# Kernel optimization log

Hardware: AMD Instinct MI355X
Metric: run time of the kernel (lower is better)

Reference implementation:

```python
import jax, jax.numpy as jnp
import numpy as np

B, OBS, H, D, E, T, A = 8192, 128, 512, 512, 16, 50, 32
LOG_STD_MIN, LOG_STD_MAX = -20.0, 2.0
ACT_LIMIT = 1.0


def setup_inputs() -> dict:
    key = jax.random.key(0)
    ks = jax.random.split(key, 24)
    s = 0.05  # weight init scale for MLP weights
    f32 = jnp.float32
    return {
        "obs": jax.random.normal(ks[0], (B, OBS), f32),
        "task": jax.random.randint(ks[1], (B,), 0, T),
        "eps": jax.random.normal(ks[2], (B, A), f32),
        # backbone: obs_dim -> 512 -> 512, relu after every layer
        "bW1": jax.random.normal(ks[3], (OBS, H), f32) * s, "bb1": jnp.zeros((H,), f32),
        "bW2": jax.random.normal(ks[4], (H, H), f32) * s, "bb2": jnp.zeros((H,), f32),
        # stacked expert MLPs: 512 -> 512(relu) -> 512(identity), batched over E
        "eW1": jax.random.normal(ks[5], (E, H, D), f32) * s, "eb1": jnp.zeros((E, D), f32),
        "eW2": jax.random.normal(ks[6], (E, D, D), f32) * s, "eb2": jnp.zeros((E, D), f32),
        # attention params (torch.randn init in original)
        "key_mats": jax.random.normal(ks[7], (E, D, D), f32),
        "value_mats": jax.random.normal(ks[8], (E, D, D), f32),
        "task_queries": jax.random.normal(ks[9], (T, D), f32),
        # mu tower: D -> 512(relu) -> act_dim
        "mW1": jax.random.normal(ks[10], (D, H), f32) * s, "mb1": jnp.zeros((H,), f32),
        "mW2": jax.random.normal(ks[11], (H, A), f32) * s, "mb2": jnp.zeros((A,), f32),
        # log_std tower: D -> 512(relu) -> act_dim
        "lW1": jax.random.normal(ks[12], (D, H), f32) * s, "lb1": jnp.zeros((H,), f32),
        "lW2": jax.random.normal(ks[13], (H, A), f32) * s, "lb2": jnp.zeros((A,), f32),
    }


def reference(obs, task, eps, bW1, bb1, bW2, bb2, eW1, eb1, eW2, eb2,
              key_mats, value_mats, task_queries,
              mW1, mb1, mW2, mb2, lW1, lb1, lW2, lb2):
    relu = jax.nn.relu
    # backbone (relu after both layers, incl. output_activation=activation)
    h = relu(obs @ bW1 + bb1)          # [B, H]
    h = relu(h @ bW2 + bb2)            # [B, H]
    # all experts as one batched GEMM (replaces jit.fork per-expert dispatch)
    eo = relu(jnp.einsum('bi,eij->bej', h, eW1) + eb1)   # [B, E, D]
    eo = jnp.einsum('bej,ejk->bek', eo, eW2) + eb2       # [B, E, D]
    # attention-weighted mixture of experts
    vals = jnp.einsum('bei,eij->bej', eo, value_mats)    # [B, E, D]
    keys = jnp.einsum('bei,eij->bej', eo, key_mats)      # [B, E, D]
    q = task_queries[task]                               # [B, D]
    w = jax.nn.softmax(jnp.einsum('bei,bi->be', keys, q), axis=-1)  # [B, E]
    tower = jnp.einsum('be,bei->bi', w, vals)            # [B, D]
    # squashed Gaussian head
    mu = relu(tower @ mW1 + mb1) @ mW2 + mb2             # [B, A]
    log_std = jnp.clip(relu(tower @ lW1 + lb1) @ lW2 + lb2, LOG_STD_MIN, LOG_STD_MAX)
    a = mu + jnp.exp(log_std) * eps                      # rsample with explicit noise
    # Normal log_prob of a = mu + std*eps, summed over action dim
    logp = jnp.sum(-0.5 * eps * eps - log_std - 0.5 * jnp.log(2.0 * jnp.pi), axis=-1)
    # tanh-squash correction
    logp = logp - jnp.sum(2.0 * (jnp.log(2.0) - a - jax.nn.softplus(-2.0 * a)), axis=-1)
    pi = ACT_LIMIT * jnp.tanh(a)
    return (pi, logp)
```

## Files before the change

kernel.cpp:

```cpp
#include <hip/hip_runtime.h>
#include <hip/hip_bf16.h>
#include <cstdint>


typedef _Float16 f16;
typedef _Float16 f16x4 __attribute__((ext_vector_type(4)));
typedef _Float16 f16x8 __attribute__((ext_vector_type(8)));
typedef float f32x4 __attribute__((ext_vector_type(4)));

__device__ __forceinline__ void fsplit(float x, f16& h, f16& l) {
    h = (f16)x;
    l = (f16)(x - (float)h);
}

__device__ __forceinline__ void gload16(const void* g, void* s) {
    __builtin_amdgcn_global_load_lds(
        (const __attribute__((address_space(1))) void*)g,
        (__attribute__((address_space(3))) void*)s, 16, 0, 0);
}

__global__ void split_pairs(const float* __restrict__ x, f16* __restrict__ h,
                            f16* __restrict__ l, int n4) {
    int i = blockIdx.x * 256 + threadIdx.x;
    if (i >= n4) return;
    float4 v = ((const float4*)x)[i];
    float a[4] = {v.x, v.y, v.z, v.w};
    f16x4 hh, ll;
#pragma unroll
    for (int j = 0; j < 4; ++j) { f16 hj, lj; fsplit(a[j], hj, lj); hh[j] = hj; ll[j] = lj; }
    *(f16x4*)&h[(long)i * 4] = hh;
    *(f16x4*)&l[(long)i * 4] = ll;
}

__global__ void transpose_split(const float* __restrict__ W, f16* __restrict__ Th,
                                f16* __restrict__ Tl, int K, int N, long ist, long ost) {
    __shared__ float t[32][33];
    const float* Wb = W + (long)blockIdx.z * ist;
    const int k0 = blockIdx.x * 32, n0 = blockIdx.y * 32;
    const int tid = threadIdx.x;
    const int r = tid >> 3, c4 = (tid & 7) * 4;
    float4 v = *(const float4*)&Wb[(long)(k0 + r) * N + n0 + c4];
    t[r][c4] = v.x; t[r][c4 + 1] = v.y; t[r][c4 + 2] = v.z; t[r][c4 + 3] = v.w;
    __syncthreads();
    f16x4 hh, ll;
#pragma unroll
    for (int j = 0; j < 4; ++j) { f16 hj, lj; fsplit(t[c4 + j][r], hj, lj); hh[j] = hj; ll[j] = lj; }
    long ob = (long)blockIdx.z * ost + (long)(n0 + r) * K + k0 + c4;
    *(f16x4*)&Th[ob] = hh;
    *(f16x4*)&Tl[ob] = ll;
}

__global__ void build_w2t(const float* __restrict__ mW2, const float* __restrict__ lW2,
                          float* __restrict__ W2T) {
    const int i = blockIdx.x * 256 + threadIdx.x;
    const int half = i >> 14, col = (i >> 9) & 31, k = i & 511;
    const float* src = half ? lW2 : mW2;
    W2T[i] = src[k * 32 + col];
}

__global__ void build_bcat(const float* __restrict__ mb1, const float* __restrict__ lb1,
                           float* __restrict__ bcat) {
    const int i = blockIdx.x * 256 + threadIdx.x;
    bcat[i] = (i < 512) ? mb1[i] : lb1[i - 512];
}

template <int OUTM, bool RELU, int AMODE, bool BSINGLE>
__global__ __launch_bounds__(256, AMODE == 0 ? 3 : 4) void gemm_pair(
    const f16* __restrict__ Ah, const f16* __restrict__ Al, int lda, long zsA,
    const f16* __restrict__ Bh, const f16* __restrict__ Bl, int ldb, long zsB,
    const float* __restrict__ bias, long zsBias,
    f16* __restrict__ Ch, f16* __restrict__ Cl, float* __restrict__ Cf,
    int ldc, long zsC, int K,
    const float* __restrict__ wscale,
    const int* __restrict__ task, const float* __restrict__ KQ2,
    float* __restrict__ scores) {
    __shared__ f16 As[AMODE == 0 ? 2 : 1][64][64];
    __shared__ f16 Bs[BSINGLE ? 1 : 2][128][64];
    const int z = blockIdx.z;
    Ah += (long)z * zsA;
    if constexpr (AMODE == 0) Al += (long)z * zsA;
    Bh += (long)z * zsB;
    if constexpr (!BSINGLE) Bl += (long)z * zsB;
    if (bias) bias += (long)z * zsBias;
    if (OUTM <= 1) { Ch += (long)z * zsC; Cl += (long)z * zsC; }
    if (OUTM == 7) { Ch += (long)z * zsC; }
    if (OUTM == 2 || OUTM == 3 || OUTM == 6) { Cf += (long)z * zsC; }
    const int tid = threadIdx.x;
    const int l = tid & 63;
    const int w = tid >> 6;
    const int row0 = blockIdx.x * 64;
    const int col0 = blockIdx.y * 128;
    const int wr = (w >> 1) * 32;
    const int wc = (w & 1) * 64;
    const int grow = l >> 3;
    const int gch = (l & 7) ^ grow;

    f32x4 acc[2][4];
#pragma unroll
    for (int mi = 0; mi < 2; ++mi)
#pragma unroll
        for (int ni = 0; ni < 4; ++ni)
#pragma unroll
            for (int j = 0; j < 4; ++j) acc[mi][ni][j] = 0.f;

    uint4 areg0, areg1; float ascl0, ascl1;
    auto ldA = [&](int k0) {
        const int r0 = w * 16 + grow, r1 = r0 + 8;
        const int scl = l & 7;
        areg0 = *(const uint4*)&Ah[(long)(row0 + r0) * lda + k0 + scl * 8];
        areg1 = *(const uint4*)&Ah[(long)(row0 + r1) * lda + k0 + scl * 8];
        const int e = k0 >> 9;
        ascl0 = wscale[(long)(row0 + r0) * 16 + e];
        ascl1 = wscale[(long)(row0 + r1) * 16 + e];
    };
    auto wrA = [&]() {
        const int scl = l & 7;
#pragma unroll
        for (int h = 0; h < 2; ++h) {
            const int r = w * 16 + grow + h * 8;
            const float s = h ? ascl1 : ascl0;
            f16x8 v = h ? *(f16x8*)&areg1 : *(f16x8*)&areg0;
#pragma unroll
            for (int j = 0; j < 8; ++j) v[j] = (f16)((float)v[j] * s);
            *(uint4*)&As[0][r][(scl ^ (r & 7)) * 8] = *(uint4*)&v;
        }
    };

    if constexpr (AMODE == 2) ldA(0);
    for (int k0 = 0; k0 < K; k0 += 64) {
        __syncthreads();
        if constexpr (AMODE == 2) {
            wrA();
            if (k0 + 64 < K) ldA(k0 + 64);
        } else {
            const long ga = (long)(row0 + w * 16 + grow) * lda + k0 + gch * 8;
            gload16(Ah + ga, &As[0][w * 16][0]);
            gload16(Ah + ga + (long)8 * lda, &As[0][w * 16 + 8][0]);
            if constexpr (AMODE == 0) {
                gload16(Al + ga, &As[1][w * 16][0]);
                gload16(Al + ga + (long)8 * lda, &As[1][w * 16 + 8][0]);
            }
        }
        {
            const long gb = (long)(col0 + w * 32 + grow) * ldb + k0 + gch * 8;
            gload16(Bh + gb, &Bs[0][w * 32][0]);
            gload16(Bh + gb + (long)8 * ldb, &Bs[0][w * 32 + 8][0]);
            gload16(Bh + gb + (long)16 * ldb, &Bs[0][w * 32 + 16][0]);
            gload16(Bh + gb + (long)24 * ldb, &Bs[0][w * 32 + 24][0]);
            if constexpr (!BSINGLE) {
                gload16(Bl + gb, &Bs[1][w * 32][0]);
                gload16(Bl + gb + (long)8 * ldb, &Bs[1][w * 32 + 8][0]);
                gload16(Bl + gb + (long)16 * ldb, &Bs[1][w * 32 + 16][0]);
                gload16(Bl + gb + (long)24 * ldb, &Bs[1][w * 32 + 24][0]);
            }
        }
        __syncthreads();
        const int r16 = l & 15, kg = l >> 4;
#pragma unroll
        for (int ks = 0; ks < 2; ++ks) {
            f16x8 a_h[2], a_l[2], b_h[4], b_l[4];
#pragma unroll
            for (int mi = 0; mi < 2; ++mi) {
                const int r = wr + mi * 16 + r16;
                const int off = ((ks * 4 + kg) ^ (r & 7)) * 8;
                a_h[mi] = *(const f16x8*)&As[0][r][off];
                if constexpr (AMODE == 0) a_l[mi] = *(const f16x8*)&As[1][r][off];
            }
#pragma unroll
            for (int ni = 0; ni < 4; ++ni) {
                const int c = wc + ni * 16 + r16;
                const int off = ((ks * 4 + kg) ^ (c & 7)) * 8;
                b_h[ni] = *(const f16x8*)&Bs[0][c][off];
                if constexpr (!BSINGLE) b_l[ni] = *(const f16x8*)&Bs[1][c][off];
            }
#pragma unroll
            for (int mi = 0; mi < 2; ++mi)
#pragma unroll
                for (int ni = 0; ni < 4; ++ni) {
                    acc[mi][ni] = __builtin_amdgcn_mfma_f32_16x16x32_f16(a_h[mi], b_h[ni], acc[mi][ni], 0, 0, 0);
                    if constexpr (!BSINGLE)
                        acc[mi][ni] = __builtin_amdgcn_mfma_f32_16x16x32_f16(a_h[mi], b_l[ni], acc[mi][ni], 0, 0, 0);
                    if constexpr (AMODE == 0)
                        acc[mi][ni] = __builtin_amdgcn_mfma_f32_16x16x32_f16(a_l[mi], b_h[ni], acc[mi][ni], 0, 0, 0);
                }
        }
    }
    const int lane15 = l & 15;
    const int rsub = (l >> 4) * 4;
    if (OUTM == 5) {
        const int expert = col0 >> 9;
        float bv[4];
#pragma unroll
        for (int ni = 0; ni < 4; ++ni)
            bv[ni] = bias ? bias[col0 + wc + ni * 16 + lane15] : 0.f;
#pragma unroll
        for (int mi = 0; mi < 2; ++mi)
#pragma unroll
            for (int j = 0; j < 4; ++j) {
                const int rowg = row0 + wr + mi * 16 + rsub + j;
                const int t = task[rowg];
                const float* kqr = KQ2 + ((long)t * 16 + expert) * 512;
                float part = 0.f;
#pragma unroll
                for (int ni = 0; ni < 4; ++ni) {
                    const int colg = col0 + wc + ni * 16 + lane15;
                    float v = acc[mi][ni][j] + bv[ni];
                    if (RELU) v = fmaxf(v, 0.f);
                    Ch[(long)rowg * ldc + colg] = (f16)v;
                    part += v * kqr[colg & 511];
                }
#pragma unroll
                for (int d = 1; d < 16; d <<= 1) part += __shfl_xor(part, d);
                if (lane15 == 0) atomicAdd(&scores[rowg * 16 + expert], part);
            }
    } else {
#pragma unroll
        for (int mi = 0; mi < 2; ++mi)
#pragma unroll
            for (int ni = 0; ni < 4; ++ni) {
                const int colg = col0 + wc + ni * 16 + lane15;
                const float bv = bias ? bias[colg] : 0.f;
#pragma unroll
                for (int j = 0; j < 4; ++j) {
                    const int rowg = row0 + wr + mi * 16 + rsub + j;
                    float v = acc[mi][ni][j] + bv;
                    if (RELU) v = fmaxf(v, 0.f);
                    if (OUTM == 0) {
                        f16 hh, ll; fsplit(v, hh, ll);
                        const long idx = (long)rowg * ldc + colg;
                        Ch[idx] = hh; Cl[idx] = ll;
                    } else if (OUTM == 1) {
                        f16 hh, ll; fsplit(v, hh, ll);
                        const long idx = (long)colg * ldc + rowg;
                        Ch[idx] = hh; Cl[idx] = ll;
                    } else if (OUTM == 2) {
                        Cf[(long)rowg * ldc + colg] = v;
                    } else if (OUTM == 3) {
                        Cf[(long)rowg * ldc + colg] += v;
                    } else if (OUTM == 6) {
                        Cf[(long)colg * ldc + rowg] = v;
                    } else if (OUTM == 7) {
                        Ch[(long)colg * ldc + rowg] = (f16)v;
                    } else if (OUTM == 8) {
                        const long idx = (long)rowg * ldc + colg;
                        v += Cf[idx];
                        Ch[idx] = (f16)v;
                    }
                }
            }
    }
}

__global__ void cb_from_kq(const f16* __restrict__ KqT_h, const f16* __restrict__ KqT_l,
                           const float* __restrict__ eb2, float* __restrict__ cb) {
    const int gw = (blockIdx.x * 256 + threadIdx.x) >> 6;
    const int l = threadIdx.x & 63;
    const int t = gw >> 4, e = gw & 15;
    const long base = (long)t * 8192 + e * 512 + l * 8;
    f16x8 hh = *(const f16x8*)&KqT_h[base];
    f16x8 ll = *(const f16x8*)&KqT_l[base];
    const float* bb = eb2 + e * 512 + l * 8;
    float s = 0.f;
#pragma unroll
    for (int j = 0; j < 8; ++j) s += ((float)hh[j] + (float)ll[j]) * bb[j];
#pragma unroll
    for (int d = 1; d < 64; d <<= 1) s += __shfl_xor(s, d);
    if (l == 0) cb[t * 16 + e] = s;
}

__global__ void bias_fold(const float* __restrict__ bvec, const float* __restrict__ M,
                          float* __restrict__ out) {
    const int gid = blockIdx.x * 256 + threadIdx.x;
    const int e = gid >> 9, j = gid & 511;
    const float* Me = M + (long)e * 262144;
    const float* be = bvec + e * 512;
    float s = 0.f;
    for (int k = 0; k < 512; ++k) s += be[k] * Me[(long)k * 512 + j];
    out[gid] = s;
}

__global__ void scores_init(const int* __restrict__ task, const float* __restrict__ cb,
                            float* __restrict__ sc) {
    const int i = blockIdx.x * 256 + threadIdx.x;
    sc[i] = cb[task[i >> 4] * 16 + (i & 15)];
}

__global__ void softmax16(float* __restrict__ sc) {
    const int b = blockIdx.x * 256 + threadIdx.x;
    float v[16];
    const float4* pp = (const float4*)&sc[b * 16];
#pragma unroll
    for (int qq = 0; qq < 4; ++qq) {
        float4 t = pp[qq];
        v[qq * 4] = t.x; v[qq * 4 + 1] = t.y; v[qq * 4 + 2] = t.z; v[qq * 4 + 3] = t.w;
    }
    float m = v[0];
#pragma unroll
    for (int e = 1; e < 16; ++e) m = fmaxf(m, v[e]);
    float ssum = 0.f;
#pragma unroll
    for (int e = 0; e < 16; ++e) { v[e] = expf(v[e] - m); ssum += v[e]; }
    const float inv = 1.f / ssum;
    float4* o = (float4*)&sc[b * 16];
#pragma unroll
    for (int qq = 0; qq < 4; ++qq) {
        float4 t;
        t.x = v[qq * 4] * inv; t.y = v[qq * 4 + 1] * inv;
        t.z = v[qq * 4 + 2] * inv; t.w = v[qq * 4 + 3] * inv;
        o[qq] = t;
    }
}

__global__ void wb_init(const float* __restrict__ w, const float* __restrict__ b2V,
                        float* __restrict__ towerAcc) {
    const int b = blockIdx.x;
    const int tid = threadIdx.x;
    float wv[16];
#pragma unroll
    for (int e = 0; e < 16; ++e) wv[e] = w[b * 16 + e];
#pragma unroll
    for (int rep = 0; rep < 2; ++rep) {
        const int j = rep * 256 + tid;
        float s = 0.f;
#pragma unroll
        for (int e = 0; e < 16; ++e) s += wv[e] * b2V[e * 512 + j];
        towerAcc[(long)b * 512 + j] = s;
    }
}

__global__ void head_kernel2(
    const f16* __restrict__ Rh, const f16* __restrict__ Rl,
    const float* __restrict__ W2T,
    const float* __restrict__ mb2, const float* __restrict__ lb2,
    const float* __restrict__ eps, float* __restrict__ pi, float* __restrict__ logp) {
    __shared__ float src[4][1032];
    const int tid = threadIdx.x, l = tid & 63, w = tid >> 6;
    const int b = blockIdx.x * 4 + w;
    const long rb = (long)b * 1024;
    {
        f16x8 h0 = *(const f16x8*)&Rh[rb + l * 8];
        f16x8 l0 = *(const f16x8*)&Rl[rb + l * 8];
        f16x8 h1 = *(const f16x8*)&Rh[rb + 512 + l * 8];
        f16x8 l1 = *(const f16x8*)&Rl[rb + 512 + l * 8];
#pragma unroll
        for (int j = 0; j < 8; ++j) {
            src[w][l * 8 + j] = (float)h0[j] + (float)l0[j];
            src[w][512 + l * 8 + j] = (float)h1[j] + (float)l1[j];
        }
    }
    __syncthreads();
    const int col = l & 31;
    const int half = l >> 5;
    const float4* wp = (const float4*)(W2T + ((long)(half * 32 + col)) * 512);
    const float4* sp = (const float4*)(&src[w][half * 512]);
    float a0 = 0.f, a1 = 0.f, a2 = 0.f, a3 = 0.f;
#pragma unroll 8
    for (int k4 = 0; k4 < 128; ++k4) {
        const float4 wv = wp[k4];
        const float4 sv = sp[k4];
        a0 = fmaf(wv.x, sv.x, a0);
        a1 = fmaf(wv.y, sv.y, a1);
        a2 = fmaf(wv.z, sv.z, a2);
        a3 = fmaf(wv.w, sv.w, a3);
    }
    const float* b2 = half ? lb2 : mb2;
    float s = b2[col] + ((a0 + a1) + (a2 + a3));
    const float other = __shfl_xor(s, 32);
    if (half == 0) {
        const float mu = s;
        float ls = fminf(fmaxf(other, -20.f), 2.f);
        const float e = eps[(long)b * 32 + col];
        const float a = mu + expf(ls) * e;
        float lt = -0.5f * e * e - ls - 0.91893853320467274f;
        const float x = -2.f * a;
        const float sp2 = fmaxf(x, 0.f) + log1pf(expf(-fabsf(x)));
        lt -= 2.f * (0.69314718055994531f - a - sp2);
        pi[(long)b * 32 + col] = tanhf(a);
        float r = lt;
#pragma unroll
        for (int d = 1; d < 32; d <<= 1) r += __shfl_xor(r, d);
        if (col == 0) logp[b] = r;
    }
}

extern "C" void kernel_launch(void* const* d_in, const int* in_sizes, int n_in,
                              void* d_out, int out_size, void* d_ws, size_t ws_size,
                              hipStream_t stream) {
    const float* obs = (const float*)d_in[0];
    const int* task = (const int*)d_in[1];
    const float* eps = (const float*)d_in[2];
    const float* bW1 = (const float*)d_in[3];
    const float* bb1 = (const float*)d_in[4];
    const float* bW2 = (const float*)d_in[5];
    const float* bb2 = (const float*)d_in[6];
    const float* eW1 = (const float*)d_in[7];
    const float* eb1 = (const float*)d_in[8];
    const float* eW2 = (const float*)d_in[9];
    const float* eb2 = (const float*)d_in[10];
    const float* keyM = (const float*)d_in[11];
    const float* valM = (const float*)d_in[12];
    const float* tq = (const float*)d_in[13];
    const float* mW1 = (const float*)d_in[14];
    const float* mb1 = (const float*)d_in[15];
    const float* mW2 = (const float*)d_in[16];
    const float* mb2 = (const float*)d_in[17];
    const float* lW1 = (const float*)d_in[18];
    const float* lb1 = (const float*)d_in[19];
    const float* lW2 = (const float*)d_in[20];
    const float* lb2 = (const float*)d_in[21];
    (void)in_sizes; (void)n_in; (void)out_size; (void)ws_size;

    const size_t MB = 1u << 20, KB = 1u << 10;
    char* base = (char*)d_ws;
    f16* eW1t_h = (f16*)(base + 0 * MB);   f16* eW1t_l = (f16*)(base + 8 * MB);
    f16* Wv2_h  = (f16*)(base + 16 * MB);
    f16* eW2s_h = (f16*)(base + 32 * MB);  f16* eW2s_l = (f16*)(base + 40 * MB);
    f16* h2_h   = (f16*)(base + 32 * MB);  f16* h2_l   = (f16*)(base + 40 * MB);
    f16* t1_h   = (f16*)(base + 48 * MB);  f16* t1_l   = (f16*)(base + 56 * MB);
    f16* Rcat_l = (f16*)(base + 48 * MB);
    f16* Vt_h   = (f16*)(base + 64 * MB);  f16* Vt_l   = (f16*)(base + 72 * MB);
    f16* Rcat_h = (f16*)(base + 64 * MB);
    f16* keyMs_h = (f16*)(base + 80 * MB); f16* keyMs_l = (f16*)(base + 88 * MB);
    f16* KqT_h   = (f16*)(base + 96 * MB); f16* KqT_l   = (f16*)(base + 98 * MB);
    f16* tqP_h   = (f16*)(base + 100 * MB); f16* tqP_l  = (f16*)(base + 100 * MB + 128 * KB);
    float* KQ2   = (float*)(base + 104 * MB);
    float* towerAcc = (float*)(base + 80 * MB);
    f16* twP_h  = (f16*)(base + 96 * MB);
    f16* obs_h  = (f16*)(base + 112 * MB); f16* obs_l  = (f16*)(base + 114 * MB);
    char* q = base + 116 * MB;
    f16* bW1t_h = (f16*)q; q += 128 * KB;  f16* bW1t_l = (f16*)q; q += 128 * KB;
    f16* bW2t_h = (f16*)q; q += 512 * KB;  f16* bW2t_l = (f16*)q; q += 512 * KB;
    f16* mW1t_h = (f16*)q; q += 512 * KB;
    f16* lW1t_h = (f16*)q; q += 512 * KB;
    f16* mW1t_l = (f16*)q; q += 512 * KB;
    f16* lW1t_l = (f16*)q; q += 512 * KB;
    float* scores = (float*)q; q += 512 * KB;
    float* b2V    = (float*)q; q += 32 * KB;
    float* cb     = (float*)q; q += 16 * KB;
    float* W2T    = (float*)q; q += 128 * KB;
    float* bcat   = (float*)q; q += 16 * KB;
    f16* U = (f16*)(base + 122 * MB);

    const long EST = 262144;

    split_pairs<<<1024, 256, 0, stream>>>(obs, obs_h, obs_l, 262144);
    split_pairs<<<4096, 256, 0, stream>>>(eW2, eW2s_h, eW2s_l, 1048576);
    split_pairs<<<4096, 256, 0, stream>>>(keyM, keyMs_h, keyMs_l, 1048576);
    hipMemsetAsync(tqP_h, 0, 256 * KB, stream);
    split_pairs<<<25, 256, 0, stream>>>(tq, tqP_h, tqP_l, 6400);
    transpose_split<<<dim3(4, 16, 1), 256, 0, stream>>>(bW1, bW1t_h, bW1t_l, 128, 512, 0, 0);
    transpose_split<<<dim3(16, 16, 1), 256, 0, stream>>>(bW2, bW2t_h, bW2t_l, 512, 512, 0, 0);
    transpose_split<<<dim3(16, 16, 1), 256, 0, stream>>>(mW1, mW1t_h, mW1t_l, 512, 512, 0, 0);
    transpose_split<<<dim3(16, 16, 1), 256, 0, stream>>>(lW1, lW1t_h, lW1t_l, 512, 512, 0, 0);
    transpose_split<<<dim3(16, 16, 16), 256, 0, stream>>>(eW1, eW1t_h, eW1t_l, 512, 512, EST, EST);
    transpose_split<<<dim3(16, 16, 16), 256, 0, stream>>>(valM, Vt_h, Vt_l, 512, 512, EST, EST);
    build_w2t<<<128, 256, 0, stream>>>(mW2, lW2, W2T);
    build_bcat<<<4, 256, 0, stream>>>(mb1, lb1, bcat);

    gemm_pair<7, false, 0, true><<<dim3(8, 4, 16), 256, 0, stream>>>(
        eW2s_h, eW2s_l, 512, EST, Vt_h, nullptr, 512, EST, nullptr, 0,
        Wv2_h, nullptr, nullptr, 8192, 512, 512, nullptr, nullptr, nullptr, nullptr);
    gemm_pair<1, false, 0, false><<<dim3(128, 1, 1), 256, 0, stream>>>(
        keyMs_h, keyMs_l, 512, 0, tqP_h, tqP_l, 512, 0, nullptr, 0,
        KqT_h, KqT_l, nullptr, 8192, 0, 512, nullptr, nullptr, nullptr, nullptr);
    gemm_pair<6, false, 0, false><<<dim3(8, 1, 16), 256, 0, stream>>>(
        eW2s_h, eW2s_l, 512, EST, KqT_h, KqT_l, 8192, 512, nullptr, 0,
        nullptr, nullptr, KQ2, 8192, 512, 512, nullptr, nullptr, nullptr, nullptr);
    cb_from_kq<<<200, 256, 0, stream>>>(KqT_h, KqT_l, eb2, cb);
    bias_fold<<<32, 256, 0, stream>>>(eb2, valM, b2V);

    gemm_pair<0, true, 0, false><<<dim3(128, 4, 1), 256, 0, stream>>>(
        obs_h, obs_l, 128, 0, bW1t_h, bW1t_l, 128, 0, bb1, 0,
        t1_h, t1_l, nullptr, 512, 0, 128, nullptr, nullptr, nullptr, nullptr);
    gemm_pair<0, true, 0, false><<<dim3(128, 4, 1), 256, 0, stream>>>(
        t1_h, t1_l, 512, 0, bW2t_h, bW2t_l, 512, 0, bb2, 0,
        h2_h, h2_l, nullptr, 512, 0, 512, nullptr, nullptr, nullptr, nullptr);

    scores_init<<<512, 256, 0, stream>>>(task, cb, scores);
    gemm_pair<5, true, 0, false><<<dim3(128, 64, 1), 256, 0, stream>>>(
        h2_h, h2_l, 512, 0, eW1t_h, eW1t_l, 512, 0, eb1, 0,
        U, nullptr, nullptr, 8192, 0, 512, nullptr, task, KQ2, scores);
    softmax16<<<32, 256, 0, stream>>>(scores);

    wb_init<<<8192, 256, 0, stream>>>(scores, b2V, towerAcc);
    gemm_pair<8, false, 2, true><<<dim3(128, 4, 1), 256, 0, stream>>>(
        U, nullptr, 8192, 0, Wv2_h, nullptr, 8192, 0, nullptr, 0,
        twP_h, nullptr, towerAcc, 512, 0, 8192, scores, nullptr, nullptr, nullptr);

    gemm_pair<0, true, 1, true><<<dim3(128, 4, 2), 256, 0, stream>>>(
        twP_h, nullptr, 512, 0, mW1t_h, nullptr, 512, 262144, bcat, 512,
        Rcat_h, Rcat_l, nullptr, 1024, 512, 512, nullptr, nullptr, nullptr, nullptr);
    head_kernel2<<<2048, 256, 0, stream>>>(Rcat_h, Rcat_l, W2T, mb2, lb2, eps,
                                           (float*)d_out, (float*)d_out + 262144);
}
```

Measured before the change: 663.9 us.

## Add dedicated 128x128 mixing GEMM, fuse prep kernels, remap expert GEMM blocks

Replaces the scaled-A mixing GEMM path (K=8192) with a dedicated mix_gemm kernel using 128x128 tiles and 4x4 MFMA per wave, giving more reuse per loaded tile. Merges the two large split launches and five transpose launches into single kernels to cut launch overhead. Remaps block indices for the expert-layer-1 GEMM so that blocks sharing B columns land on the same XCD, aiming at better L2 locality. The mixing grid shrinks to 256 blocks, which may reduce occupancy, and the larger accumulator adds register pressure.

```diff
diff --git a/kernel.cpp b/kernel.cpp
--- a/kernel.cpp
+++ b/kernel.cpp
@@ -30,6 +30,22 @@
     for (int j = 0; j < 4; ++j) { f16 hj, lj; fsplit(a[j], hj, lj); hh[j] = hj; ll[j] = lj; }
     *(f16x4*)&h[(long)i * 4] = hh;
     *(f16x4*)&l[(long)i * 4] = ll;
+}
+
+__global__ void split_pairs2(const float* __restrict__ xa, f16* __restrict__ ha,
+                             f16* __restrict__ la, const float* __restrict__ xb,
+                             f16* __restrict__ hb, f16* __restrict__ lb) {
+    long i = (long)blockIdx.x * 256 + threadIdx.x;
+    const float* x; f16* h; f16* l;
+    if (i < 1048576) { x = xa; h = ha; l = la; }
+    else { i -= 1048576; x = xb; h = hb; l = lb; }
+    float4 v = ((const float4*)x)[i];
+    float a[4] = {v.x, v.y, v.z, v.w};
+    f16x4 hh, ll;
+#pragma unroll
+    for (int j = 0; j < 4; ++j) { f16 hj, lj; fsplit(a[j], hj, lj); hh[j] = hj; ll[j] = lj; }
+    *(f16x4*)&h[i * 4] = hh;
+    *(f16x4*)&l[i * 4] = ll;
 }
 
 __global__ void transpose_split(const float* __restrict__ W, f16* __restrict__ Th,
@@ -50,6 +66,37 @@
     *(f16x4*)&Tl[ob] = ll;
 }
 
+__global__ void transpose_split5(
+    const float* __restrict__ eW1, const float* __restrict__ valM,
+    const float* __restrict__ bW2, const float* __restrict__ mW1,
+    const float* __restrict__ lW1,
+    f16* __restrict__ eW1t_h, f16* __restrict__ eW1t_l,
+    f16* __restrict__ Vt_h, f16* __restrict__ Vt_l,
+    f16* __restrict__ bW2t_h, f16* __restrict__ bW2t_l,
+    f16* __restrict__ mW1t_h, f16* __restrict__ mW1t_l,
+    f16* __restrict__ lW1t_h, f16* __restrict__ lW1t_l) {
+    __shared__ float t[32][33];
+    const int z = blockIdx.z;
+    const float* W; f16* Th; f16* Tl;
+    if (z < 16) { W = eW1 + (long)z * 262144; Th = eW1t_h + (long)z * 262144; Tl = eW1t_l + (long)z * 262144; }
+    else if (z < 32) { const int e = z - 16; W = valM + (long)e * 262144; Th = Vt_h + (long)e * 262144; Tl = Vt_l + (long)e * 262144; }
+    else if (z == 32) { W = bW2; Th = bW2t_h; Tl = bW2t_l; }
+    else if (z == 33) { W = mW1; Th = mW1t_h; Tl = mW1t_l; }
+    else { W = lW1; Th = lW1t_h; Tl = lW1t_l; }
+    const int k0 = blockIdx.x * 32, n0 = blockIdx.y * 32;
+    const int tid = threadIdx.x;
+    const int r = tid >> 3, c4 = (tid & 7) * 4;
+    float4 v = *(const float4*)&W[(long)(k0 + r) * 512 + n0 + c4];
+    t[r][c4] = v.x; t[r][c4 + 1] = v.y; t[r][c4 + 2] = v.z; t[r][c4 + 3] = v.w;
+    __syncthreads();
+    f16x4 hh, ll;
+#pragma unroll
+    for (int j = 0; j < 4; ++j) { f16 hj, lj; fsplit(t[c4 + j][r], hj, lj); hh[j] = hj; ll[j] = lj; }
+    const long ob = (long)(n0 + r) * 512 + k0 + c4;
+    *(f16x4*)&Th[ob] = hh;
+    *(f16x4*)&Tl[ob] = ll;
+}
+
 __global__ void build_w2t(const float* __restrict__ mW2, const float* __restrict__ lW2,
                           float* __restrict__ W2T) {
     const int i = blockIdx.x * 256 + threadIdx.x;
@@ -71,7 +118,6 @@
     const float* __restrict__ bias, long zsBias,
     f16* __restrict__ Ch, f16* __restrict__ Cl, float* __restrict__ Cf,
     int ldc, long zsC, int K,
-    const float* __restrict__ wscale,
     const int* __restrict__ task, const float* __restrict__ KQ2,
     float* __restrict__ scores) {
     __shared__ f16 As[AMODE == 0 ? 2 : 1][64][64];
@@ -88,8 +134,15 @@
     const int tid = threadIdx.x;
     const int l = tid & 63;
     const int w = tid >> 6;
-    const int row0 = blockIdx.x * 64;
-    const int col0 = blockIdx.y * 128;
+    int bx = blockIdx.x, by = blockIdx.y;
+    if constexpr (OUTM == 5) {
+        const int id = by * gridDim.x + bx;
+        const int xcd = id & 7, r = id >> 3;
+        by = (xcd << 3) | (r & 7);
+        bx = r >> 3;
+    }
+    const int row0 = bx * 64;
+    const int col0 = by * 128;
     const int wr = (w >> 1) * 32;
     const int wc = (w & 1) * 64;
     const int grow = l >> 3;
@@ -103,36 +156,9 @@
 #pragma unroll
             for (int j = 0; j < 4; ++j) acc[mi][ni][j] = 0.f;
 
-    uint4 areg0, areg1; float ascl0, ascl1;
-    auto ldA = [&](int k0) {
-        const int r0 = w * 16 + grow, r1 = r0 + 8;
-        const int scl = l & 7;
-        areg0 = *(const uint4*)&Ah[(long)(row0 + r0) * lda + k0 + scl * 8];
-        areg1 = *(const uint4*)&Ah[(long)(row0 + r1) * lda + k0 + scl * 8];
-        const int e = k0 >> 9;
-        ascl0 = wscale[(long)(row0 + r0) * 16 + e];
-        ascl1 = wscale[(long)(row0 + r1) * 16 + e];
-    };
-    auto wrA = [&]() {
-        const int scl = l & 7;
-#pragma unroll
-        for (int h = 0; h < 2; ++h) {
-            const int r = w * 16 + grow + h * 8;
-            const float s = h ? ascl1 : ascl0;
-            f16x8 v = h ? *(f16x8*)&areg1 : *(f16x8*)&areg0;
-#pragma unroll
-            for (int j = 0; j < 8; ++j) v[j] = (f16)((float)v[j] * s);
-            *(uint4*)&As[0][r][(scl ^ (r & 7)) * 8] = *(uint4*)&v;
-        }
-    };
-
-    if constexpr (AMODE == 2) ldA(0);
     for (int k0 = 0; k0 < K; k0 += 64) {
         __syncthreads();
-        if constexpr (AMODE == 2) {
-            wrA();
-            if (k0 + 64 < K) ldA(k0 + 64);
-        } else {
+        {
             const long ga = (long)(row0 + w * 16 + grow) * lda + k0 + gch * 8;
             gload16(Ah + ga, &As[0][w * 16][0]);
             gload16(Ah + ga + (long)8 * lda, &As[0][w * 16 + 8][0]);
@@ -140,8 +166,6 @@
                 gload16(Al + ga, &As[1][w * 16][0]);
                 gload16(Al + ga + (long)8 * lda, &As[1][w * 16 + 8][0]);
             }
-        }
-        {
             const long gb = (long)(col0 + w * 32 + grow) * ldb + k0 + gch * 8;
             gload16(Bh + gb, &Bs[0][w * 32][0]);
             gload16(Bh + gb + (long)8 * ldb, &Bs[0][w * 32 + 8][0]);
@@ -249,6 +273,101 @@
                 }
             }
     }
+}
+
+__global__ __launch_bounds__(256, 4) void mix_gemm(
+    const f16* __restrict__ U, int lda,
+    const f16* __restrict__ Bh, int ldb,
+    const float* __restrict__ wscale,
+    const float* __restrict__ wb,
+    f16* __restrict__ Co, int ldc, int K) {
+    __shared__ f16 As[128][64];
+    __shared__ f16 Bs[128][64];
+    const int tid = threadIdx.x;
+    const int l = tid & 63, w = tid >> 6;
+    const int row0 = blockIdx.x * 128, col0 = blockIdx.y * 128;
+    const int wr = (w >> 1) * 64, wc = (w & 1) * 64;
+    const int grow = l >> 3;
+    const int scl = l & 7;
+    const int gch = scl ^ grow;
+
+    f32x4 acc[4][4];
+#pragma unroll
+    for (int mi = 0; mi < 4; ++mi)
+#pragma unroll
+        for (int ni = 0; ni < 4; ++ni)
+#pragma unroll
+            for (int j = 0; j < 4; ++j) acc[mi][ni][j] = 0.f;
+
+    uint4 areg[4]; float ascl[4];
+    auto ldA = [&](int k0) {
+        const int e = k0 >> 9;
+#pragma unroll
+        for (int i = 0; i < 4; ++i) {
+            const int r = w * 32 + i * 8 + grow;
+            areg[i] = *(const uint4*)&U[(long)(row0 + r) * lda + k0 + scl * 8];
+            ascl[i] = wscale[(long)(row0 + r) * 16 + e];
+        }
+    };
+    auto wrA = [&]() {
+#pragma unroll
+        for (int i = 0; i < 4; ++i) {
+            const int r = w * 32 + i * 8 + grow;
+            f16x8 v = *(f16x8*)&areg[i];
+#pragma unroll
+            for (int jj = 0; jj < 8; ++jj) v[jj] = (f16)((float)v[jj] * ascl[i]);
+            *(uint4*)&As[r][(scl ^ (r & 7)) * 8] = *(uint4*)&v;
+        }
+    };
+
+    ldA(0);
+    for (int k0 = 0; k0 < K; k0 += 64) {
+        __syncthreads();
+        wrA();
+        if (k0 + 64 < K) ldA(k0 + 64);
+        {
+            const long gb = (long)(col0 + w * 32 + grow) * ldb + k0 + gch * 8;
+            gload16(Bh + gb, &Bs[w * 32][0]);
+            gload16(Bh + gb + (long)8 * ldb, &Bs[w * 32 + 8][0]);
+            gload16(Bh + gb + (long)16 * ldb, &Bs[w * 32 + 16][0]);
+            gload16(Bh + gb + (long)24 * ldb, &Bs[w * 32 + 24][0]);
+        }
+        __syncthreads();
+        const int r16 = l & 15, kg = l >> 4;
+#pragma unroll
+        for (int ks = 0; ks < 2; ++ks) {
+            f16x8 a[4], b[4];
+#pragma unroll
+            for (int mi = 0; mi < 4; ++mi) {
+                const int r = wr + mi * 16 + r16;
+                a[mi] = *(const f16x8*)&As[r][(((ks * 4 + kg) ^ (r & 7)) * 8)];
+            }
+#pragma unroll
+            for (int ni = 0; ni < 4; ++ni) {
+                const int c = wc + ni * 16 + r16;
+                b[ni] = *(const f16x8*)&Bs[c][(((ks * 4 + kg) ^ (c & 7)) * 8)];
+            }
+#pragma unroll
+            for (int mi = 0; mi < 4; ++mi)
+#pragma unroll
+                for (int ni = 0; ni < 4; ++ni)
+                    acc[mi][ni] = __builtin_amdgcn_mfma_f32_16x16x32_f16(a[mi], b[ni], acc[mi][ni], 0, 0, 0);
+        }
+    }
+    const int lane15 = l & 15;
+    const int rsub = (l >> 4) * 4;
+#pragma unroll
+    for (int mi = 0; mi < 4; ++mi)
+#pragma unroll
+        for (int ni = 0; ni < 4; ++ni) {
+            const int colg = col0 + wc + ni * 16 + lane15;
+#pragma unroll
+            for (int j = 0; j < 4; ++j) {
+                const int rowg = row0 + wr + mi * 16 + rsub + j;
+                const long idx = (long)rowg * ldc + colg;
+                Co[idx] = (f16)(acc[mi][ni][j] + wb[idx]);
+            }
+        }
 }
 
 __global__ void cb_from_kq(const f16* __restrict__ KqT_h, const f16* __restrict__ KqT_l,
@@ -444,52 +563,48 @@
     const long EST = 262144;
 
     split_pairs<<<1024, 256, 0, stream>>>(obs, obs_h, obs_l, 262144);
-    split_pairs<<<4096, 256, 0, stream>>>(eW2, eW2s_h, eW2s_l, 1048576);
-    split_pairs<<<4096, 256, 0, stream>>>(keyM, keyMs_h, keyMs_l, 1048576);
+    split_pairs2<<<8192, 256, 0, stream>>>(eW2, eW2s_h, eW2s_l, keyM, keyMs_h, keyMs_l);
     hipMemsetAsync(tqP_h, 0, 256 * KB, stream);
     split_pairs<<<25, 256, 0, stream>>>(tq, tqP_h, tqP_l, 6400);
     transpose_split<<<dim3(4, 16, 1), 256, 0, stream>>>(bW1, bW1t_h, bW1t_l, 128, 512, 0, 0);
-    transpose_split<<<dim3(16, 16, 1), 256, 0, stream>>>(bW2, bW2t_h, bW2t_l, 512, 512, 0, 0);
-    transpose_split<<<dim3(16, 16, 1), 256, 0, stream>>>(mW1, mW1t_h, mW1t_l, 512, 512, 0, 0);
-    transpose_split<<<dim3(16, 16, 1), 256, 0, stream>>>(lW1, lW1t_h, lW1t_l, 512, 512, 0, 0);
-    transpose_split<<<dim3(16, 16, 16), 256, 0, stream>>>(eW1, eW1t_h, eW1t_l, 512, 512, EST, EST);
-    transpose_split<<<dim3(16, 16, 16), 256, 0, stream>>>(valM, Vt_h, Vt_l, 512, 512, EST, EST);
+    transpose_split5<<<dim3(16, 16, 35), 256, 0, stream>>>(
+        eW1, valM, bW2, mW1, lW1, eW1t_h, eW1t_l, Vt_h, Vt_l,
+        bW2t_h, bW2t_l, mW1t_h, mW1t_l, lW1t_h, lW1t_l);
     build_w2t<<<128, 256, 0, stream>>>(mW2, lW2, W2T);
     build_bcat<<<4, 256, 0, stream>>>(mb1, lb1, bcat);
 
     gemm_pair<7, false, 0, true><<<dim3(8, 4, 16), 256, 0, stream>>>(
         eW2s_h, eW2s_l, 512, EST, Vt_h, nullptr, 512, EST, nullptr, 0,
-        Wv2_h, nullptr, nullptr, 8192, 512, 512, nullptr, nullptr, nullptr, nullptr);
+        Wv2_h, nullptr, nullptr, 8192, 512, 512, nullptr, nullptr, nullptr);
     gemm_pair<1, false, 0, false><<<dim3(128, 1, 1), 256, 0, stream>>>(
         keyMs_h, keyMs_l, 512, 0, tqP_h, tqP_l, 512, 0, nullptr, 0,
-        KqT_h, KqT_l, nullptr, 8192, 0, 512, nullptr, nullptr, nullptr, nullptr);
+        KqT_h, KqT_l, nullptr, 8192, 0, 512, nullptr, nullptr, nullptr);
     gemm_pair<6, false, 0, false><<<dim3(8, 1, 16), 256, 0, stream>>>(
         eW2s_h, eW2s_l, 512, EST, KqT_h, KqT_l, 8192, 512, nullptr, 0,
-        nullptr, nullptr, KQ2, 8192, 512, 512, nullptr, nullptr, nullptr, nullptr);
+        nullptr, nullptr, KQ2, 8192, 512, 512, nullptr, nullptr, nullptr);
     cb_from_kq<<<200, 256, 0, stream>>>(KqT_h, KqT_l, eb2, cb);
     bias_fold<<<32, 256, 0, stream>>>(eb2, valM, b2V);
 
     gemm_pair<0, true, 0, false><<<dim3(128, 4, 1), 256, 0, stream>>>(
         obs_h, obs_l, 128, 0, bW1t_h, bW1t_l, 128, 0, bb1, 0,
-        t1_h, t1_l, nullptr, 512, 0, 128, nullptr, nullptr, nullptr, nullptr);
+        t1_h, t1_l, nullptr, 512, 0, 128, nullptr, nullptr, nullptr);
     gemm_pair<0, true, 0, false><<<dim3(128, 4, 1), 256, 0, stream>>>(
         t1_h, t1_l, 512, 0, bW2t_h, bW2t_l, 512, 0, bb2, 0,
-        h2_h, h2_l, nullptr, 512, 0, 512, nullptr, nullptr, nullptr, nullptr);
+        h2_h, h2_l, nullptr, 512, 0, 512, nullptr, nullptr, nullptr);
 
     scores_init<<<512, 256, 0, stream>>>(task, cb, scores);
     gemm_pair<5, true, 0, false><<<dim3(128, 64, 1), 256, 0, stream>>>(
         h2_h, h2_l, 512, 0, eW1t_h, eW1t_l, 512, 0, eb1, 0,
-        U, nullptr, nullptr, 8192, 0, 512, nullptr, task, KQ2, scores);
+        U, nullptr, nullptr, 8192, 0, 512, task, KQ2, scores);
     softmax16<<<32, 256, 0, stream>>>(scores);
 
     wb_init<<<8192, 256, 0, stream>>>(scores, b2V, towerAcc);
-    gemm_pair<8, false, 2, true><<<dim3(128, 4, 1), 256, 0, stream>>>(
-        U, nullptr, 8192, 0, Wv2_h, nullptr, 8192, 0, nullptr, 0,
-        twP_h, nullptr, towerAcc, 512, 0, 8192, scores, nullptr, nullptr, nullptr);
+    mix_gemm<<<dim3(64, 4, 1), 256, 0, stream>>>(
+        U, 8192, Wv2_h, 8192, scores, towerAcc, twP_h, 512, 8192);
 
     gemm_pair<0, true, 1, true><<<dim3(128, 4, 2), 256, 0, stream>>>(
         twP_h, nullptr, 512, 0, mW1t_h, nullptr, 512, 262144, bcat, 512,
-        Rcat_h, Rcat_l, nullptr, 1024, 512, 512, nullptr, nullptr, nullptr, nullptr);
+        Rcat_h, Rcat_l, nullptr, 1024, 512, 512, nullptr, nullptr, nullptr);
     head_kernel2<<<2048, 256, 0, stream>>>(Rcat_h, Rcat_l, W2T, mb2, lb2, eps,
                                            (float*)d_out, (float*)d_out + 262144);
 }
```

New measurement: 738.6 us. 11.2% more time.
